# Optimization experiments

Hardware: AMD Instinct MI355X
Metric: run time of the kernel (lower is better)

## Reference

```python
import jax, jax.numpy as jnp
import numpy as np

SP = 4
HEADS = 4
LN_EPS = 1e-4


def _branch(q, k, v, h, hsp, w, wsp, lepe_w, lepe_b, scale, heads):
    # q,k,v: [B, L, Cb] with spatial layout (h hsp w wsp), channel layout (c head)
    B = q.shape[0]
    Cb = q.shape[-1]
    c = Cb // heads

    def win(t):
        t = t.reshape(B, h, hsp, w, wsp, c, heads)
        t = t.transpose(0, 1, 3, 6, 2, 4, 5)  # B,h,w,head,hsp,wsp,c
        return t.reshape(B * h * w, heads, hsp * wsp, c)

    q, k, v = win(q), win(k), win(v)
    Bw = B * h * w
    # LePE: depthwise 3x3 conv on v in image layout [(b h w), (c head), hsp, wsp]
    vimg = v.reshape(Bw, heads, hsp, wsp, c).transpose(0, 4, 1, 2, 3).reshape(Bw, Cb, hsp, wsp)
    lepe = jax.lax.conv_general_dilated(
        vimg, lepe_w, window_strides=(1, 1), padding='SAME',
        dimension_numbers=('NCHW', 'OIHW', 'NCHW'), feature_group_count=Cb)
    lepe = lepe + lepe_b[None, :, None, None]
    lepe = lepe.reshape(Bw, c, heads, hsp, wsp).transpose(0, 2, 3, 4, 1).reshape(Bw, heads, hsp * wsp, c)
    # stripe-window attention
    attn = jax.nn.softmax((q * scale) @ jnp.swapaxes(k, -2, -1), axis=-1)
    o = attn @ v + lepe
    # back to image: [(b h w), head, (hsp wsp), c] -> [B, (c head), (h hsp), (w wsp)]
    o = o.reshape(B, h, w, heads, hsp, wsp, c).transpose(0, 6, 3, 1, 4, 2, 5)
    o = o.reshape(B, Cb, h * hsp, w * wsp)
    return o, attn


def reference(x, ln_g, ln_b, w_qkv, proj_w, proj_b, lepe_w1, lepe_b1, lepe_w2, lepe_b2):
    B, C, H, W = x.shape
    heads, sp = HEADS, SP
    scale = (C // heads) ** (-0.5)  # scale uses full dim // num_heads as in __init__
    # [B,C,H,W] -> [B, H*W, C], LayerNorm over C
    xp = x.transpose(0, 2, 3, 1).reshape(B, H * W, C)
    mu = xp.mean(-1, keepdims=True)
    var = xp.var(-1, keepdims=True)
    xn = (xp - mu) * jax.lax.rsqrt(var + LN_EPS) * ln_g + ln_b
    qkv = xn @ w_qkv.T  # [B, L, 3C]
    q, k, v = jnp.split(qkv, 3, axis=-1)
    Ch = C // 2
    # branch 1: vertical stripes (full H, width sp); branch 2: horizontal stripes
    params = [(1, H, W // sp, sp, lepe_w1, lepe_b1),
              (H // sp, sp, 1, W, lepe_w2, lepe_b2)]
    outs, attns = [], []
    for i, (h, hsp, w, wsp, lw, lb) in enumerate(params):
        sl = slice(i * Ch, (i + 1) * Ch)
        o, a = _branch(q[..., sl], k[..., sl], v[..., sl], h, hsp, w, wsp, lw, lb, scale, heads)
        outs.append(o)
        attns.append(a)
    xcat = jnp.concatenate(outs, axis=1)  # [B, C, H, W]
    out = jnp.einsum('bchw,oc->bohw', xcat, proj_w[:, :, 0, 0]) + proj_b[None, :, None, None]
    return (out, attns[0], attns[1])


def setup_inputs() -> dict:
    key = jax.random.key(0)
    ks = jax.random.split(key, 6)
    B, C, H, W = 8, 256, 64, 64
    return {
        'x': jax.random.normal(ks[0], (B, C, H, W), dtype=jnp.float32),
        'ln_g': jnp.ones((C,), jnp.float32),
        'ln_b': jnp.zeros((C,), jnp.float32),
        'w_qkv': jax.random.normal(ks[1], (3 * C, C), dtype=jnp.float32) * 0.02,
        'proj_w': jax.random.normal(ks[2], (C, C, 1, 1), dtype=jnp.float32) * 0.02,
        'proj_b': jnp.zeros((C,), jnp.float32),
        'lepe_w1': jax.random.normal(ks[3], (C // 2, 1, 3, 3), dtype=jnp.float32) * 0.1,
        'lepe_b1': jnp.zeros((C // 2,), jnp.float32),
        'lepe_w2': jax.random.normal(ks[4], (C // 2, 1, 3, 3), dtype=jnp.float32) * 0.1,
        'lepe_b2': jnp.zeros((C // 2,), jnp.float32),
    }
```

## Files before the change

kernel.cpp:

```cpp
#include <hip/hip_runtime.h>
#include <math.h>

typedef short bf8 __attribute__((ext_vector_type(8)));
typedef float f4  __attribute__((ext_vector_type(4)));

__device__ inline float b2f(unsigned short u) {
    return __uint_as_float(((unsigned int)u) << 16);
}
__device__ inline unsigned short f2b(float f) {
    unsigned int u = __float_as_uint(f);
    u = (u + 0x7fffu + ((u >> 16) & 1u)) >> 16;
    return (unsigned short)u;
}

__global__ __launch_bounds__(256) void k_ln_t(const float* __restrict__ x,
                                              const float* __restrict__ g,
                                              const float* __restrict__ beta,
                                              unsigned short* __restrict__ xnb) {
    __shared__ float xt[32 * 261];
    __shared__ float ps[8][32];
    __shared__ float ps2[8][32];
    __shared__ float ms[32];
    __shared__ float rs[32];
    int l0 = blockIdx.x * 32, b = blockIdx.y;
    int tid = threadIdx.x;
    int tl = tid & 31, c0 = tid >> 5;
    const float* xb = x + (size_t)b * 1048576 + l0 + tl;
    float s = 0.f, s2 = 0.f;
#pragma unroll 8
    for (int rr = 0; rr < 32; ++rr) {
        int c = rr * 8 + c0;
        float v = xb[(size_t)c * 4096];
        int cm = c ^ (((rr >> 2) & 7) << 2);
        xt[tl * 261 + cm] = v;
        s += v; s2 += v * v;
    }
    ps[c0][tl] = s; ps2[c0][tl] = s2;
    __syncthreads();
    if (tid < 32) {
        float t = 0.f, t2 = 0.f;
#pragma unroll
        for (int j = 0; j < 8; ++j) { t += ps[j][tid]; t2 += ps2[j][tid]; }
        float m = t * (1.f / 256.f);
        float var = t2 * (1.f / 256.f) - m * m;
        ms[tid] = m;
        rs[tid] = rsqrtf(var + 1e-4f);
    }
    __syncthreads();
    int lw = tid >> 3, cc = (tid & 7) * 32;
    int xr = (tid & 7) << 2;
    float m = ms[lw], r = rs[lw];
    unsigned short* dst = xnb + ((size_t)b * 4096 + l0 + lw) * 256 + cc;
#pragma unroll
    for (int q4 = 0; q4 < 4; ++q4) {
        int cb = cc + q4 * 8;
        float gv[8], bv[8];
        *(float4*)(gv)     = *(const float4*)(g + cb);
        *(float4*)(gv + 4) = *(const float4*)(g + cb + 4);
        *(float4*)(bv)     = *(const float4*)(beta + cb);
        *(float4*)(bv + 4) = *(const float4*)(beta + cb + 4);
        union { unsigned short u[8]; uint4 v; } pk;
#pragma unroll
        for (int e = 0; e < 8; ++e) {
            int cm = (cb + e) ^ xr;
            pk.u[e] = f2b((xt[lw * 261 + cm] - m) * r * gv[e] + bv[e]);
        }
        *(uint4*)(dst + q4 * 8) = pk.v;
    }
}

__global__ __launch_bounds__(256) void k_wcvt(const float* __restrict__ w,
                                              unsigned short* __restrict__ wb) {
    int i = (blockIdx.x * 256 + threadIdx.x) * 8;
    float4 a = *(const float4*)(w + i);
    float4 c = *(const float4*)(w + i + 4);
    union { unsigned short u[8]; uint4 v; } r;
    r.u[0] = f2b(a.x); r.u[1] = f2b(a.y); r.u[2] = f2b(a.z); r.u[3] = f2b(a.w);
    r.u[4] = f2b(c.x); r.u[5] = f2b(c.y); r.u[6] = f2b(c.z); r.u[7] = f2b(c.w);
    *(uint4*)(wb + i) = r.v;
}

__global__ __launch_bounds__(256) void k_qkv(const unsigned short* __restrict__ wb,
                                             const unsigned short* __restrict__ xnb,
                                             unsigned short* __restrict__ qw,
                                             unsigned short* __restrict__ kw,
                                             unsigned short* __restrict__ vw) {
    int jt = blockIdx.x, lt = blockIdx.y, b = blockIdx.z;
    int tid = threadIdx.x;
    int w = tid >> 6, lane = tid & 63;
    int ln15 = lane & 15, quad = lane >> 4;
    const unsigned short* A = wb + (size_t)jt * 64 * 256 + ln15 * 256 + quad * 8;
    const unsigned short* B = xnb + ((size_t)b * 4096 + lt * 256 + w * 64 + ln15) * 256 + quad * 8;
    const f4 z = {0.f, 0.f, 0.f, 0.f};
    f4 acc[4][4];
#pragma unroll
    for (int i = 0; i < 4; i++)
#pragma unroll
        for (int j = 0; j < 4; j++) acc[i][j] = z;
#pragma unroll 2
    for (int k0 = 0; k0 < 256; k0 += 32) {
        bf8 af[4], bvf[4];
#pragma unroll
        for (int i = 0; i < 4; i++) af[i]  = *(const bf8*)(A + i * 16 * 256 + k0);
#pragma unroll
        for (int j = 0; j < 4; j++) bvf[j] = *(const bf8*)(B + j * 16 * 256 + k0);
#pragma unroll
        for (int i = 0; i < 4; i++)
#pragma unroll
            for (int j = 0; j < 4; j++)
                acc[i][j] = __builtin_amdgcn_mfma_f32_16x16x32_bf16(af[i], bvf[j], acc[i][j], 0, 0, 0);
    }
    int lbase = lt * 256 + w * 64;
#pragma unroll
    for (int i = 0; i < 4; i++) {
#pragma unroll
        for (int r = 0; r < 4; r++) {
            int j = jt * 64 + i * 16 + quad * 4 + r;
            int sel = j >> 8;
            int jr = j & 255;
            int branch = jr >> 7;
            int chb = jr & 127;
            int d = chb >> 2, head = chb & 3;
            unsigned short* dst = (sel == 0) ? qw : ((sel == 1) ? kw : vw);
            float sc = (sel == 0) ? 0.125f : 1.f;
#pragma unroll
            for (int jf = 0; jf < 4; jf++) {
                int ll = lbase + jf * 16 + ln15;
                int row = ll >> 6, col = ll & 63;
                int win, pos;
                if (branch == 0) { win = col >> 2; pos = (row << 2) | (col & 3); }
                else             { win = row >> 2; pos = ((row & 3) << 6) | col; }
                int bw = b * 16 + win;
                size_t idx;
                if (sel == 2)
                    idx = ((((size_t)branch * 128 + bw) * 4 + head) * 32 + d) * 256 + pos;
                else
                    idx = ((((size_t)branch * 128 + bw) * 4 + head) * 256 + pos) * 32 + d;
                dst[idx] = f2b(acc[i][jf][r] * sc);
            }
        }
    }
}

__global__ __launch_bounds__(256, 3) void k_attn(const unsigned short* __restrict__ qw,
                                                 const unsigned short* __restrict__ kw,
                                                 const unsigned short* __restrict__ vw,
                                                 const float* __restrict__ lw1,
                                                 const float* __restrict__ lb1,
                                                 const float* __restrict__ lw2,
                                                 const float* __restrict__ lb2,
                                                 float* __restrict__ attn_out,
                                                 float* __restrict__ xcat) {
    __shared__ __align__(16) char smem[49792];
    float*          olds = (float*)smem;
    unsigned short* vt   = (unsigned short*)(smem + 32896);

    int bid = blockIdx.x;
    int branch = bid >> 9;
    int bw = (bid >> 2) & 127;
    int head = bid & 3;
    int tid = threadIdx.x;
    int w = tid >> 6, lane = tid & 63;
    int ln15 = lane & 15, quad = lane >> 4;
    int rowbase = w * 64;

    size_t base = (((size_t)branch * 128 + bw) * 4 + head) * 8192;
    const unsigned short* qb = qw + base;
    const unsigned short* kb = kw + base;
    const unsigned short* vb = vw + base;

    {
        int d = tid >> 3, ck = (tid & 7) * 32;
        const uint4* s = (const uint4*)(vb + d * 256 + ck);
        uint4* dst = (uint4*)(vt + d * 264 + ck);
        dst[0] = s[0]; dst[1] = s[1]; dst[2] = s[2]; dst[3] = s[3];
    }

    bf8 qf[4];
#pragma unroll
    for (int rt = 0; rt < 4; rt++)
        qf[rt] = *(const bf8*)(qb + (rowbase + rt * 16 + ln15) * 32 + quad * 8);

    const f4 z = {0.f, 0.f, 0.f, 0.f};

    f4 lsum[4] = {z, z, z, z};
    for (int jtile = 0; jtile < 16; jtile++) {
        bf8 kf = *(const bf8*)(kb + (jtile * 16 + ln15) * 32 + quad * 8);
#pragma unroll
        for (int rt = 0; rt < 4; rt++) {
            f4 s = __builtin_amdgcn_mfma_f32_16x16x32_bf16(qf[rt], kf, z, 0, 0, 0);
            lsum[rt].x += __expf(s.x);
            lsum[rt].y += __expf(s.y);
            lsum[rt].z += __expf(s.z);
            lsum[rt].w += __expf(s.w);
        }
    }
    f4 inv[4];
#pragma unroll
    for (int rt = 0; rt < 4; rt++) {
        float a0 = lsum[rt].x, a1 = lsum[rt].y, a2 = lsum[rt].z, a3 = lsum[rt].w;
#pragma unroll
        for (int m = 1; m < 16; m <<= 1) {
            a0 += __shfl_xor(a0, m); a1 += __shfl_xor(a1, m);
            a2 += __shfl_xor(a2, m); a3 += __shfl_xor(a3, m);
        }
        inv[rt].x = 1.f / a0; inv[rt].y = 1.f / a1;
        inv[rt].z = 1.f / a2; inv[rt].w = 1.f / a3;
    }

    __syncthreads();

    unsigned short* plw = ((unsigned short*)olds) + w * 512;
    float* abase = attn_out + (size_t)branch * 33554432ull
                 + ((size_t)(bw * 4 + head)) * 65536;
    f4 oacc[4][2] = {{z, z}, {z, z}, {z, z}, {z, z}};
    for (int t = 0; t < 8; t++) {
        int c0 = t * 32;
        bf8 kf0 = *(const bf8*)(kb + (c0 + ln15) * 32 + quad * 8);
        bf8 kf1 = *(const bf8*)(kb + (c0 + 16 + ln15) * 32 + quad * 8);
        bf8 vf0 = *(const bf8*)(vt + ln15 * 264 + c0 + quad * 8);
        bf8 vf1 = *(const bf8*)(vt + (16 + ln15) * 264 + c0 + quad * 8);
#pragma unroll
        for (int rt = 0; rt < 4; rt++) {
            f4 s0 = __builtin_amdgcn_mfma_f32_16x16x32_bf16(qf[rt], kf0, z, 0, 0, 0);
            f4 s1 = __builtin_amdgcn_mfma_f32_16x16x32_bf16(qf[rt], kf1, z, 0, 0, 0);
            f4 p0, p1;
            p0.x = __expf(s0.x) * inv[rt].x; p0.y = __expf(s0.y) * inv[rt].y;
            p0.z = __expf(s0.z) * inv[rt].z; p0.w = __expf(s0.w) * inv[rt].w;
            p1.x = __expf(s1.x) * inv[rt].x; p1.y = __expf(s1.y) * inv[rt].y;
            p1.z = __expf(s1.z) * inv[rt].z; p1.w = __expf(s1.w) * inv[rt].w;
            float* ar = abase + (size_t)(rowbase + rt * 16 + quad * 4) * 256 + c0 + ln15;
            ar[0]   = p0.x; ar[256] = p0.y; ar[512] = p0.z; ar[768] = p0.w;
            ar[16]  = p1.x; ar[272] = p1.y; ar[528] = p1.z; ar[784] = p1.w;
            plw[(quad * 4 + 0) * 32 + ln15]      = f2b(p0.x);
            plw[(quad * 4 + 1) * 32 + ln15]      = f2b(p0.y);
            plw[(quad * 4 + 2) * 32 + ln15]      = f2b(p0.z);
            plw[(quad * 4 + 3) * 32 + ln15]      = f2b(p0.w);
            plw[(quad * 4 + 0) * 32 + 16 + ln15] = f2b(p1.x);
            plw[(quad * 4 + 1) * 32 + 16 + ln15] = f2b(p1.y);
            plw[(quad * 4 + 2) * 32 + 16 + ln15] = f2b(p1.z);
            plw[(quad * 4 + 3) * 32 + 16 + ln15] = f2b(p1.w);
            bf8 pf = *(const bf8*)(plw + ln15 * 32 + quad * 8);
            oacc[rt][0] = __builtin_amdgcn_mfma_f32_16x16x32_bf16(pf, vf0, oacc[rt][0], 0, 0, 0);
            oacc[rt][1] = __builtin_amdgcn_mfma_f32_16x16x32_bf16(pf, vf1, oacc[rt][1], 0, 0, 0);
        }
    }

    __syncthreads();
#pragma unroll
    for (int rt = 0; rt < 4; rt++)
#pragma unroll
        for (int dt = 0; dt < 2; dt++) {
            int d = dt * 16 + ln15;
            int r = rowbase + rt * 16 + quad * 4;
            olds[d * 257 + r + 0] = oacc[rt][dt][0];
            olds[d * 257 + r + 1] = oacc[rt][dt][1];
            olds[d * 257 + r + 2] = oacc[rt][dt][2];
            olds[d * 257 + r + 3] = oacc[rt][dt][3];
        }
    __syncthreads();

    const float* lw = branch ? lw2 : lw1;
    const float* lb = branch ? lb2 : lb1;
    int p = tid;
    int hs, ws_;
    if (branch == 0) { hs = p >> 2; ws_ = p & 3; }
    else             { hs = p >> 6; ws_ = p & 63; }
    int win = bw & 15, b = bw >> 4;
    int row, col;
    if (branch == 0) { row = p >> 2; col = (win << 2) | (p & 3); }
    else             { row = (win << 2) | (p >> 6); col = p & 63; }
    size_t lpix = (size_t)row * 64 + col;
#pragma unroll
    for (int d = 0; d < 32; ++d) {
        float acc = lb[d * 4 + head];
#pragma unroll
        for (int ky = 0; ky < 3; ky++) {
#pragma unroll
            for (int kx = 0; kx < 3; kx++) {
                int ny = hs + ky - 1, nx = ws_ + kx - 1;
                bool ok; int np;
                if (branch == 0) { ok = (ny >= 0 && ny < 64 && nx >= 0 && nx < 4);  np = (ny << 2) | (nx & 3); }
                else             { ok = (ny >= 0 && ny < 4  && nx >= 0 && nx < 64); np = (ny << 6) | (nx & 63); }
                if (ok) acc += lw[(d * 4 + head) * 9 + ky * 3 + kx] * b2f(vt[d * 264 + np]);
            }
        }
        float oval = olds[d * 257 + p] + acc;
        int chg = branch * 128 + d * 4 + head;
        xcat[((size_t)b * 256 + chg) * 4096 + lpix] = oval;
    }
}

__global__ __launch_bounds__(256) void k_proj(const float* __restrict__ pw,
                                              const float* __restrict__ pb,
                                              const float* __restrict__ xcat,
                                              float* __restrict__ out) {
    __shared__ float sA[16][68];
    __shared__ float sB[16][68];
    int jt = blockIdx.x, lt = blockIdx.y, b = blockIdx.z;
    int j0 = jt * 64, l0 = lt * 64;
    int tid = threadIdx.x;
    float acc[4][4] = {};
    int ar = tid >> 2, ac4 = (tid & 3) << 2;
    int tl = tid & 63;
    for (int k0 = 0; k0 < 256; k0 += 16) {
        float4 av = *(const float4*)(pw + (size_t)(j0 + ar) * 256 + k0 + ac4);
        sA[ac4 + 0][ar] = av.x; sA[ac4 + 1][ar] = av.y;
        sA[ac4 + 2][ar] = av.z; sA[ac4 + 3][ar] = av.w;
#pragma unroll
        for (int i = 0; i < 4; i++) {
            int kr = (tid >> 6) + i * 4;
            sB[kr][tl] = xcat[((size_t)b * 256 + k0 + kr) * 4096 + l0 + tl];
        }
        __syncthreads();
#pragma unroll
        for (int kk = 0; kk < 16; ++kk) {
            float4 a4 = *(const float4*)&sA[kk][(tid >> 4) << 2];
            float4 b4 = *(const float4*)&sB[kk][(tid & 15) << 2];
            acc[0][0] += a4.x * b4.x; acc[0][1] += a4.x * b4.y; acc[0][2] += a4.x * b4.z; acc[0][3] += a4.x * b4.w;
            acc[1][0] += a4.y * b4.x; acc[1][1] += a4.y * b4.y; acc[1][2] += a4.y * b4.z; acc[1][3] += a4.y * b4.w;
            acc[2][0] += a4.z * b4.x; acc[2][1] += a4.z * b4.y; acc[2][2] += a4.z * b4.z; acc[2][3] += a4.z * b4.w;
            acc[3][0] += a4.w * b4.x; acc[3][1] += a4.w * b4.y; acc[3][2] += a4.w * b4.z; acc[3][3] += a4.w * b4.w;
        }
        __syncthreads();
    }
#pragma unroll
    for (int i = 0; i < 4; i++) {
        int jj = j0 + ((tid >> 4) << 2) + i;
        float bias = pb[jj];
        float4 r4;
        r4.x = acc[i][0] + bias; r4.y = acc[i][1] + bias;
        r4.z = acc[i][2] + bias; r4.w = acc[i][3] + bias;
        *(float4*)(out + ((size_t)b * 256 + jj) * 4096 + l0 + ((tid & 15) << 2)) = r4;
    }
}

extern "C" void kernel_launch(void* const* d_in, const int* in_sizes, int n_in,
                              void* d_out, int out_size, void* d_ws, size_t ws_size,
                              hipStream_t stream) {
    const float* x    = (const float*)d_in[0];
    const float* ln_g = (const float*)d_in[1];
    const float* ln_b = (const float*)d_in[2];
    const float* wqkv = (const float*)d_in[3];
    const float* pw   = (const float*)d_in[4];
    const float* pb   = (const float*)d_in[5];
    const float* lw1  = (const float*)d_in[6];
    const float* lb1  = (const float*)d_in[7];
    const float* lw2  = (const float*)d_in[8];
    const float* lb2  = (const float*)d_in[9];

    float* ws = (float*)d_ws;
    unsigned short* xnb = (unsigned short*)(ws + 65536);
    unsigned short* wb  = xnb + 8388608;
    unsigned short* qw  = (unsigned short*)(ws + 65536 + 8388608);
    unsigned short* kw  = qw + 8388608;
    unsigned short* vw  = kw + 8388608;
    float* xcat = ws + 65536;
    float* out  = (float*)d_out;
    float* attn = out + 8388608;

    k_wcvt<<<96, 256, 0, stream>>>(wqkv, wb);
    k_ln_t<<<dim3(128, 8), 256, 0, stream>>>(x, ln_g, ln_b, xnb);
    k_qkv<<<dim3(12, 16, 8), 256, 0, stream>>>(wb, xnb, qw, kw, vw);
    k_attn<<<1024, 256, 0, stream>>>(qw, kw, vw, lw1, lb1, lw2, lb2, attn, xcat);
    k_proj<<<dim3(4, 64, 8), 256, 0, stream>>>(pw, pb, xcat, out);
}
```

Baseline: 549.7 us.

## Store xcat as bf16 pixel-major and run projection on bf16 MFMA

Result: faster. 518.6 us (-5.7%).

```diff
diff --git a/kernel.cpp b/kernel.cpp
--- a/kernel.cpp
+++ b/kernel.cpp
@@ -80,6 +80,15 @@
     *(uint4*)(wb + i) = r.v;
 }
 
+__global__ __launch_bounds__(256) void k_pcvt(const float* __restrict__ pw,
+                                              unsigned short* __restrict__ pwb) {
+    int idx = blockIdx.x * 256 + threadIdx.x;
+    int o = idx >> 8, cp = idx & 255;
+    int br = cp >> 7, head = (cp >> 5) & 3, d = cp & 31;
+    int c = br * 128 + d * 4 + head;
+    pwb[idx] = f2b(pw[o * 256 + c]);
+}
+
 __global__ __launch_bounds__(256) void k_qkv(const unsigned short* __restrict__ wb,
                                              const unsigned short* __restrict__ xnb,
                                              unsigned short* __restrict__ qw,
@@ -150,7 +159,7 @@
                                                  const float* __restrict__ lw2,
                                                  const float* __restrict__ lb2,
                                                  float* __restrict__ attn_out,
-                                                 float* __restrict__ xcat) {
+                                                 unsigned short* __restrict__ xcat) {
     __shared__ __align__(16) char smem[49792];
     float*          olds = (float*)smem;
     unsigned short* vt   = (unsigned short*)(smem + 32896);
@@ -271,67 +280,74 @@
     if (branch == 0) { row = p >> 2; col = (win << 2) | (p & 3); }
     else             { row = (win << 2) | (p >> 6); col = p & 63; }
     size_t lpix = (size_t)row * 64 + col;
-#pragma unroll
-    for (int d = 0; d < 32; ++d) {
-        float acc = lb[d * 4 + head];
-#pragma unroll
-        for (int ky = 0; ky < 3; ky++) {
-#pragma unroll
-            for (int kx = 0; kx < 3; kx++) {
-                int ny = hs + ky - 1, nx = ws_ + kx - 1;
-                bool ok; int np;
-                if (branch == 0) { ok = (ny >= 0 && ny < 64 && nx >= 0 && nx < 4);  np = (ny << 2) | (nx & 3); }
-                else             { ok = (ny >= 0 && ny < 4  && nx >= 0 && nx < 64); np = (ny << 6) | (nx & 63); }
-                if (ok) acc += lw[(d * 4 + head) * 9 + ky * 3 + kx] * b2f(vt[d * 264 + np]);
+    unsigned short* xd = xcat + (((size_t)b * 4096 + lpix) * 256) + branch * 128 + head * 32;
+#pragma unroll
+    for (int dg = 0; dg < 4; ++dg) {
+        union { unsigned short u[8]; uint4 v; } pk;
+#pragma unroll
+        for (int dd = 0; dd < 8; ++dd) {
+            int d = dg * 8 + dd;
+            float acc = lb[d * 4 + head];
+#pragma unroll
+            for (int ky = 0; ky < 3; ky++) {
+#pragma unroll
+                for (int kx = 0; kx < 3; kx++) {
+                    int ny = hs + ky - 1, nx = ws_ + kx - 1;
+                    bool ok; int np;
+                    if (branch == 0) { ok = (ny >= 0 && ny < 64 && nx >= 0 && nx < 4);  np = (ny << 2) | (nx & 3); }
+                    else             { ok = (ny >= 0 && ny < 4  && nx >= 0 && nx < 64); np = (ny << 6) | (nx & 63); }
+                    if (ok) acc += lw[(d * 4 + head) * 9 + ky * 3 + kx] * b2f(vt[d * 264 + np]);
+                }
             }
-        }
-        float oval = olds[d * 257 + p] + acc;
-        int chg = branch * 128 + d * 4 + head;
-        xcat[((size_t)b * 256 + chg) * 4096 + lpix] = oval;
-    }
-}
-
-__global__ __launch_bounds__(256) void k_proj(const float* __restrict__ pw,
+            pk.u[dd] = f2b(olds[d * 257 + p] + acc);
+        }
+        *(uint4*)(xd + dg * 8) = pk.v;
+    }
+}
+
+__global__ __launch_bounds__(256) void k_proj(const unsigned short* __restrict__ pwb,
                                               const float* __restrict__ pb,
-                                              const float* __restrict__ xcat,
+                                              const unsigned short* __restrict__ xcat,
                                               float* __restrict__ out) {
-    __shared__ float sA[16][68];
-    __shared__ float sB[16][68];
     int jt = blockIdx.x, lt = blockIdx.y, b = blockIdx.z;
-    int j0 = jt * 64, l0 = lt * 64;
     int tid = threadIdx.x;
-    float acc[4][4] = {};
-    int ar = tid >> 2, ac4 = (tid & 3) << 2;
-    int tl = tid & 63;
-    for (int k0 = 0; k0 < 256; k0 += 16) {
-        float4 av = *(const float4*)(pw + (size_t)(j0 + ar) * 256 + k0 + ac4);
-        sA[ac4 + 0][ar] = av.x; sA[ac4 + 1][ar] = av.y;
-        sA[ac4 + 2][ar] = av.z; sA[ac4 + 3][ar] = av.w;
-#pragma unroll
-        for (int i = 0; i < 4; i++) {
-            int kr = (tid >> 6) + i * 4;
-            sB[kr][tl] = xcat[((size_t)b * 256 + k0 + kr) * 4096 + l0 + tl];
-        }
-        __syncthreads();
-#pragma unroll
-        for (int kk = 0; kk < 16; ++kk) {
-            float4 a4 = *(const float4*)&sA[kk][(tid >> 4) << 2];
-            float4 b4 = *(const float4*)&sB[kk][(tid & 15) << 2];
-            acc[0][0] += a4.x * b4.x; acc[0][1] += a4.x * b4.y; acc[0][2] += a4.x * b4.z; acc[0][3] += a4.x * b4.w;
-            acc[1][0] += a4.y * b4.x; acc[1][1] += a4.y * b4.y; acc[1][2] += a4.y * b4.z; acc[1][3] += a4.y * b4.w;
-            acc[2][0] += a4.z * b4.x; acc[2][1] += a4.z * b4.y; acc[2][2] += a4.z * b4.z; acc[2][3] += a4.z * b4.w;
-            acc[3][0] += a4.w * b4.x; acc[3][1] += a4.w * b4.y; acc[3][2] += a4.w * b4.z; acc[3][3] += a4.w * b4.w;
-        }
-        __syncthreads();
-    }
+    int w = tid >> 6, lane = tid & 63;
+    int ln15 = lane & 15, quad = lane >> 4;
+    const unsigned short* A = pwb + (size_t)jt * 64 * 256 + ln15 * 256 + quad * 8;
+    const unsigned short* B = xcat + ((size_t)b * 4096 + lt * 256 + w * 64 + ln15) * 256 + quad * 8;
+    const f4 z = {0.f, 0.f, 0.f, 0.f};
+    f4 acc[4][4];
+#pragma unroll
+    for (int i = 0; i < 4; i++)
+#pragma unroll
+        for (int j = 0; j < 4; j++) acc[i][j] = z;
+#pragma unroll 2
+    for (int k0 = 0; k0 < 256; k0 += 32) {
+        bf8 af[4], bvf[4];
+#pragma unroll
+        for (int i = 0; i < 4; i++) af[i]  = *(const bf8*)(A + i * 16 * 256 + k0);
+#pragma unroll
+        for (int j = 0; j < 4; j++) bvf[j] = *(const bf8*)(B + j * 16 * 256 + k0);
+#pragma unroll
+        for (int i = 0; i < 4; i++)
+#pragma unroll
+            for (int j = 0; j < 4; j++)
+                acc[i][j] = __builtin_amdgcn_mfma_f32_16x16x32_bf16(af[i], bvf[j], acc[i][j], 0, 0, 0);
+    }
+    int lbase = lt * 256 + w * 64;
 #pragma unroll
     for (int i = 0; i < 4; i++) {
-        int jj = j0 + ((tid >> 4) << 2) + i;
-        float bias = pb[jj];
-        float4 r4;
-        r4.x = acc[i][0] + bias; r4.y = acc[i][1] + bias;
-        r4.z = acc[i][2] + bias; r4.w = acc[i][3] + bias;
-        *(float4*)(out + ((size_t)b * 256 + jj) * 4096 + l0 + ((tid & 15) << 2)) = r4;
+#pragma unroll
+        for (int r = 0; r < 4; r++) {
+            int j = jt * 64 + i * 16 + quad * 4 + r;
+            float bias = pb[j];
+            float* orow = out + ((size_t)b * 256 + j) * 4096;
+#pragma unroll
+            for (int jf = 0; jf < 4; jf++) {
+                int ll = lbase + jf * 16 + ln15;
+                orow[ll] = acc[i][jf][r] + bias;
+            }
+        }
     }
 }
 
@@ -352,16 +368,18 @@
     float* ws = (float*)d_ws;
     unsigned short* xnb = (unsigned short*)(ws + 65536);
     unsigned short* wb  = xnb + 8388608;
+    unsigned short* pwb = wb + 196608;
     unsigned short* qw  = (unsigned short*)(ws + 65536 + 8388608);
     unsigned short* kw  = qw + 8388608;
     unsigned short* vw  = kw + 8388608;
-    float* xcat = ws + 65536;
+    unsigned short* xcat = xnb;
     float* out  = (float*)d_out;
     float* attn = out + 8388608;
 
     k_wcvt<<<96, 256, 0, stream>>>(wqkv, wb);
+    k_pcvt<<<256, 256, 0, stream>>>(pw, pwb);
     k_ln_t<<<dim3(128, 8), 256, 0, stream>>>(x, ln_g, ln_b, xnb);
     k_qkv<<<dim3(12, 16, 8), 256, 0, stream>>>(wb, xnb, qw, kw, vw);
     k_attn<<<1024, 256, 0, stream>>>(qw, kw, vw, lw1, lb1, lw2, lb2, attn, xcat);
-    k_proj<<<dim3(4, 64, 8), 256, 0, stream>>>(pw, pb, xcat, out);
-}
+    k_proj<<<dim3(4, 16, 8), 256, 0, stream>>>(pwb, pb, xcat, out);
+}
```
